# Kernel optimization log

Hardware: AMD Instinct MI355X
Metric: run time of the kernel (lower is better)

Reference implementation:

```python
import jax, jax.numpy as jnp
import numpy as np

N_NODES = 150000   # node_num
N_CENTROIDS = 256  # in_feats (must equal out_feats per source view())
EMBED = 256        # out_feats
EPS = 1e-7


def setup_inputs() -> dict:
    key = jax.random.key(0)
    k1, k2, k3 = jax.random.split(key, 3)
    x = jax.random.normal(k1, (N_NODES, EMBED), dtype=jnp.float32)
    # project node representations strictly inside the unit Poincare ball
    x = x / (1.0 + jnp.linalg.norm(x, axis=-1, keepdims=True)) * 0.9
    mask = (jax.random.uniform(k2, (N_NODES, 1)) < 0.9).astype(jnp.float32)
    # centroid_embedding init: uniform(-0.01, 0.01), already well inside the ball
    w = jax.random.uniform(k3, (N_CENTROIDS, EMBED), minval=-0.01, maxval=0.01,
                           dtype=jnp.float32)
    return {"node_repr": x, "mask": mask, "centroid_weight": w}


def _poincare_pairwise(x, c):
    # x: [N, D] inside unit ball, c: [C, D] inside unit ball -> [N, C]
    sx = jnp.sum(x * x, axis=-1)              # [N]
    sc = jnp.sum(c * c, axis=-1)              # [C]
    xc = x @ c.T                               # [N, C] (the only GEMM)
    sq = jnp.maximum(sx[:, None] + sc[None, :] - 2.0 * xc, 0.0)  # ||x-y||^2
    denom = jnp.maximum((1.0 - sx)[:, None] * (1.0 - sc)[None, :], 1e-12)
    arg = 1.0 + 2.0 * sq / denom
    return jnp.arccosh(jnp.maximum(arg, 1.0 + EPS))


def reference(node_repr, mask, centroid_weight):
    # node_repr: [N, D], mask: [N, 1], centroid_weight: [C, D]
    d = _poincare_pairwise(node_repr, centroid_weight)     # [N, C]
    node_centroid_dist = d[None, :, :] * mask              # [1, N, C] (mask broadcasts)
    graph_centroid_dist = jnp.sum(node_centroid_dist, axis=1) / jnp.sum(mask)  # [1, C]
    return graph_centroid_dist, node_centroid_dist
```

## Files before the change

kernel.cpp:

```cpp
#include <hip/hip_runtime.h>
#include <hip/hip_bf16.h>

#define N_NODES 150000
#define CDIM 256
#define DIM 256

typedef float f32x4 __attribute__((ext_vector_type(4)));
typedef short bf16x8 __attribute__((ext_vector_type(8)));
typedef unsigned short u16x4 __attribute__((ext_vector_type(4)));

#define WS_CB 0
#define WS_SC 131072
#define WS_GACC 132096
#define WS_MSUM 133120

__device__ __forceinline__ unsigned short f2bf(float f) {
  unsigned u = __float_as_uint(f);
  u += 0x7FFFu + ((u >> 16) & 1u);
  return (unsigned short)(u >> 16);
}

__global__ void cd_prep(const float* __restrict__ cw, const float* __restrict__ mask,
                        unsigned short* __restrict__ cb, float* __restrict__ sc,
                        float* __restrict__ msum) {
  int b = blockIdx.x;
  int t = threadIdx.x;
  int wave = t >> 6, lane = t & 63;
  __shared__ float red[4];
  if (b < CDIM) {
    float v = cw[b * DIM + t];
    cb[(size_t)(t >> 3) * (CDIM * 8) + b * 8 + (t & 7)] = f2bf(v);
    float ss = v * v;
    #pragma unroll
    for (int off = 32; off >= 1; off >>= 1) ss += __shfl_xor(ss, off);
    if (lane == 0) red[wave] = ss;
    __syncthreads();
    if (t == 0) sc[b] = red[0] + red[1] + red[2] + red[3];
  } else {
    int idx = (b - CDIM) * 256 + t;
    const int stride = 64 * 256;
    float s = 0.f;
    for (int i = idx; i < N_NODES; i += stride) s += mask[i];
    #pragma unroll
    for (int off = 32; off >= 1; off >>= 1) s += __shfl_xor(s, off);
    if (lane == 0) red[wave] = s;
    __syncthreads();
    if (t == 0) atomicAdd(msum, red[0] + red[1] + red[2] + red[3]);
  }
}

__global__ __launch_bounds__(256, 4)
void cd_main(const float* __restrict__ x, const float* __restrict__ mask,
             const unsigned short* __restrict__ cb, const float* __restrict__ sc,
             float* __restrict__ gacc, float* __restrict__ out1) {
  __shared__ unsigned short ab[32 * 64 * 8];
  __shared__ float sxl[64];

  const int t = threadIdx.x;
  const long m0 = (long)blockIdx.x * 64;

  {
    const int row = t >> 2;
    const int qq  = t & 3;
    const long grow = m0 + row;
    const bool ok = grow < N_NODES;
    const float* px = x + grow * DIM;
    float ss = 0.f;
    #pragma unroll
    for (int i = 0; i < 16; ++i) {
      const int col4 = qq * 4 + i * 16;
      f32x4 v;
      if (ok) v = *(const f32x4*)(px + col4);
      else    v = f32x4{0.f, 0.f, 0.f, 0.f};
      ss = fmaf(v.x, v.x, ss); ss = fmaf(v.y, v.y, ss);
      ss = fmaf(v.z, v.z, ss); ss = fmaf(v.w, v.w, ss);
      u16x4 b;
      b[0] = f2bf(v.x); b[1] = f2bf(v.y); b[2] = f2bf(v.z); b[3] = f2bf(v.w);
      *(u16x4*)(ab + ((size_t)(col4 >> 3) * 64 + row) * 8 + (col4 & 7)) = b;
    }
    ss += __shfl_xor(ss, 1);
    ss += __shfl_xor(ss, 2);
    if (qq == 0) sxl[row] = ss;
  }
  __syncthreads();

  const int lane = t & 63;
  const int w = t >> 6;
  const int q = lane >> 4;
  const int ln = lane & 15;
  const int c0 = w * 64;

  f32x4 acc[4][4] = {};
  #pragma unroll
  for (int kt = 0; kt < 8; ++kt) {
    bf16x8 bf[4];
    #pragma unroll
    for (int nt = 0; nt < 4; ++nt)
      bf[nt] = *(const bf16x8*)(cb + (size_t)(kt * 4 + q) * (CDIM * 8) + (c0 + nt * 16 + ln) * 8);
    #pragma unroll
    for (int mt = 0; mt < 4; ++mt) {
      bf16x8 af = *(const bf16x8*)(ab + ((size_t)(kt * 4 + q) * 64 + mt * 16 + ln) * 8);
      #pragma unroll
      for (int nt = 0; nt < 4; ++nt)
        acc[mt][nt] = __builtin_amdgcn_mfma_f32_16x16x32_bf16(af, bf[nt], acc[mt][nt], 0, 0, 0);
    }
  }

  float scv[4], rcv[4];
  #pragma unroll
  for (int nt = 0; nt < 4; ++nt) {
    scv[nt] = sc[c0 + nt * 16 + ln];
    rcv[nt] = 1.0f - scv[nt];
  }

  float pc[4] = {0.f, 0.f, 0.f, 0.f};
  #pragma unroll
  for (int mt = 0; mt < 4; ++mt) {
    float sxe[4], rxe[4], mke[4];
    long rows[4];
    #pragma unroll
    for (int i = 0; i < 4; ++i) {
      const int rloc = q * 4 + i;
      sxe[i] = sxl[mt * 16 + rloc];
      rows[i] = m0 + mt * 16 + rloc;
      mke[i] = (rows[i] < N_NODES) ? mask[rows[i]] : 0.f;
      rxe[i] = 1.0f - sxe[i];
    }
    #pragma unroll
    for (int nt = 0; nt < 4; ++nt) {
      const int col = c0 + nt * 16 + ln;
      #pragma unroll
      for (int i = 0; i < 4; ++i) {
        float xc = acc[mt][nt][i];
        float sq = fmaf(-2.0f, xc, sxe[i] + scv[nt]);
        sq = fmaxf(sq, 0.0f);
        float den = fmaxf(rxe[i] * rcv[nt], 1e-12f);
        float z = 1.0f + __fdividef(2.0f * sq, den);
        z = fmaxf(z, 1.0f + 1e-7f);
        float t2 = z + sqrtf(fmaf(z, z, -1.0f));
        float dd = __log2f(t2) * 0.6931471805599453f;
        float o = dd * mke[i];
        if (rows[i] < N_NODES) out1[rows[i] * CDIM + col] = o;
        pc[nt] += o;
      }
    }
  }

  #pragma unroll
  for (int nt = 0; nt < 4; ++nt) {
    float s = pc[nt];
    s += __shfl_xor(s, 16);
    s += __shfl_xor(s, 32);
    if (lane < 16) atomicAdd(gacc + c0 + nt * 16 + ln, s);
  }
}

__global__ void cd_final(const float* __restrict__ gacc, const float* __restrict__ msum,
                         float* __restrict__ out0) {
  int t = threadIdx.x;
  out0[t] = gacc[t] / msum[0];
}

extern "C" void kernel_launch(void* const* d_in, const int* in_sizes, int n_in,
                              void* d_out, int out_size, void* d_ws, size_t ws_size,
                              hipStream_t stream) {
  const float* x    = (const float*)d_in[0];
  const float* mask = (const float*)d_in[1];
  const float* cw   = (const float*)d_in[2];
  float* out = (float*)d_out;
  char* ws = (char*)d_ws;
  unsigned short* cb = (unsigned short*)(ws + WS_CB);
  float* sc   = (float*)(ws + WS_SC);
  float* gacc = (float*)(ws + WS_GACC);
  float* msum = (float*)(ws + WS_MSUM);

  hipMemsetAsync(ws + WS_GACC, 0, 256 * 4 + 4, stream);
  cd_prep<<<320, 256, 0, stream>>>(cw, mask, cb, sc, msum);
  const int nblocks = (N_NODES + 63) / 64;
  cd_main<<<nblocks, 256, 0, stream>>>(x, mask, cb, sc, gacc, out + 256);
  cd_final<<<1, 256, 0, stream>>>(gacc, msum, out);
}
```

Before: 327.9 us.

## Shrink row tile to 32, prefetch centroid fragments, precompute reciprocal denominators

```diff
diff --git a/kernel.cpp b/kernel.cpp
--- a/kernel.cpp
+++ b/kernel.cpp
@@ -4,6 +4,7 @@
 #define N_NODES 150000
 #define CDIM 256
 #define DIM 256
+#define BM 32
 
 typedef float f32x4 __attribute__((ext_vector_type(4)));
 typedef short bf16x8 __attribute__((ext_vector_type(8)));
@@ -11,8 +12,9 @@
 
 #define WS_CB 0
 #define WS_SC 131072
-#define WS_GACC 132096
-#define WS_MSUM 133120
+#define WS_RC2 132096
+#define WS_GACC 133120
+#define WS_MSUM 134144
 
 __device__ __forceinline__ unsigned short f2bf(float f) {
   unsigned u = __float_as_uint(f);
@@ -22,7 +24,7 @@
 
 __global__ void cd_prep(const float* __restrict__ cw, const float* __restrict__ mask,
                         unsigned short* __restrict__ cb, float* __restrict__ sc,
-                        float* __restrict__ msum) {
+                        float* __restrict__ rc2, float* __restrict__ msum) {
   int b = blockIdx.x;
   int t = threadIdx.x;
   int wave = t >> 6, lane = t & 63;
@@ -35,7 +37,11 @@
     for (int off = 32; off >= 1; off >>= 1) ss += __shfl_xor(ss, off);
     if (lane == 0) red[wave] = ss;
     __syncthreads();
-    if (t == 0) sc[b] = red[0] + red[1] + red[2] + red[3];
+    if (t == 0) {
+      float s = red[0] + red[1] + red[2] + red[3];
+      sc[b] = s;
+      rc2[b] = 2.0f / (1.0f - s);
+    }
   } else {
     int idx = (b - CDIM) * 256 + t;
     const int stride = 64 * 256;
@@ -52,35 +58,43 @@
 __global__ __launch_bounds__(256, 4)
 void cd_main(const float* __restrict__ x, const float* __restrict__ mask,
              const unsigned short* __restrict__ cb, const float* __restrict__ sc,
-             float* __restrict__ gacc, float* __restrict__ out1) {
-  __shared__ unsigned short ab[32 * 64 * 8];
-  __shared__ float sxl[64];
+             const float* __restrict__ rc2, float* __restrict__ gacc,
+             float* __restrict__ out1) {
+  __shared__ unsigned short ab[32 * BM * 8];
+  __shared__ float sxl[BM];
+  __shared__ float mskl[BM];
 
   const int t = threadIdx.x;
-  const long m0 = (long)blockIdx.x * 64;
+  const long m0 = (long)blockIdx.x * BM;
 
   {
-    const int row = t >> 2;
-    const int qq  = t & 3;
+    const int row = t >> 3;
+    const int sub = t & 7;
     const long grow = m0 + row;
     const bool ok = grow < N_NODES;
-    const float* px = x + grow * DIM;
+    const float* px = x + grow * DIM + sub * 4;
+    f32x4 v[8];
+    #pragma unroll
+    for (int i = 0; i < 8; ++i)
+      v[i] = ok ? *(const f32x4*)(px + i * 32) : f32x4{0.f, 0.f, 0.f, 0.f};
     float ss = 0.f;
     #pragma unroll
-    for (int i = 0; i < 16; ++i) {
-      const int col4 = qq * 4 + i * 16;
-      f32x4 v;
-      if (ok) v = *(const f32x4*)(px + col4);
-      else    v = f32x4{0.f, 0.f, 0.f, 0.f};
-      ss = fmaf(v.x, v.x, ss); ss = fmaf(v.y, v.y, ss);
-      ss = fmaf(v.z, v.z, ss); ss = fmaf(v.w, v.w, ss);
+    for (int i = 0; i < 8; ++i) {
+      ss = fmaf(v[i].x, v[i].x, ss); ss = fmaf(v[i].y, v[i].y, ss);
+      ss = fmaf(v[i].z, v[i].z, ss); ss = fmaf(v[i].w, v[i].w, ss);
       u16x4 b;
-      b[0] = f2bf(v.x); b[1] = f2bf(v.y); b[2] = f2bf(v.z); b[3] = f2bf(v.w);
-      *(u16x4*)(ab + ((size_t)(col4 >> 3) * 64 + row) * 8 + (col4 & 7)) = b;
+      b[0] = f2bf(v[i].x); b[1] = f2bf(v[i].y);
+      b[2] = f2bf(v[i].z); b[3] = f2bf(v[i].w);
+      const int kf = (sub >> 1) + i * 4;
+      *(u16x4*)(ab + ((size_t)kf * BM + row) * 8 + (sub & 1) * 4) = b;
     }
     ss += __shfl_xor(ss, 1);
     ss += __shfl_xor(ss, 2);
-    if (qq == 0) sxl[row] = ss;
+    ss += __shfl_xor(ss, 4);
+    if (sub == 0) {
+      sxl[row] = ss;
+      mskl[row] = ok ? mask[grow] : 0.f;
+    }
   }
   __syncthreads();
 
@@ -90,41 +104,52 @@
   const int ln = lane & 15;
   const int c0 = w * 64;
 
-  f32x4 acc[4][4] = {};
+  bf16x8 bfc[4], bfn[4];
+  #pragma unroll
+  for (int nt = 0; nt < 4; ++nt)
+    bfc[nt] = *(const bf16x8*)(cb + (size_t)q * (CDIM * 8) + (c0 + nt * 16 + ln) * 8);
+
+  f32x4 acc[2][4] = {};
   #pragma unroll
   for (int kt = 0; kt < 8; ++kt) {
-    bf16x8 bf[4];
-    #pragma unroll
-    for (int nt = 0; nt < 4; ++nt)
-      bf[nt] = *(const bf16x8*)(cb + (size_t)(kt * 4 + q) * (CDIM * 8) + (c0 + nt * 16 + ln) * 8);
-    #pragma unroll
-    for (int mt = 0; mt < 4; ++mt) {
-      bf16x8 af = *(const bf16x8*)(ab + ((size_t)(kt * 4 + q) * 64 + mt * 16 + ln) * 8);
+    if (kt < 7) {
       #pragma unroll
       for (int nt = 0; nt < 4; ++nt)
-        acc[mt][nt] = __builtin_amdgcn_mfma_f32_16x16x32_bf16(af, bf[nt], acc[mt][nt], 0, 0, 0);
-    }
-  }
-
-  float scv[4], rcv[4];
+        bfn[nt] = *(const bf16x8*)(cb + (size_t)((kt + 1) * 4 + q) * (CDIM * 8) + (c0 + nt * 16 + ln) * 8);
+    }
+    bf16x8 af0 = *(const bf16x8*)(ab + ((size_t)(kt * 4 + q) * BM + ln) * 8);
+    bf16x8 af1 = *(const bf16x8*)(ab + ((size_t)(kt * 4 + q) * BM + 16 + ln) * 8);
+    #pragma unroll
+    for (int nt = 0; nt < 4; ++nt)
+      acc[0][nt] = __builtin_amdgcn_mfma_f32_16x16x32_bf16(af0, bfc[nt], acc[0][nt], 0, 0, 0);
+    #pragma unroll
+    for (int nt = 0; nt < 4; ++nt)
+      acc[1][nt] = __builtin_amdgcn_mfma_f32_16x16x32_bf16(af1, bfc[nt], acc[1][nt], 0, 0, 0);
+    if (kt < 7) {
+      #pragma unroll
+      for (int nt = 0; nt < 4; ++nt) bfc[nt] = bfn[nt];
+    }
+  }
+
+  float scv[4], rc2v[4];
   #pragma unroll
   for (int nt = 0; nt < 4; ++nt) {
     scv[nt] = sc[c0 + nt * 16 + ln];
-    rcv[nt] = 1.0f - scv[nt];
+    rc2v[nt] = rc2[c0 + nt * 16 + ln];
   }
 
   float pc[4] = {0.f, 0.f, 0.f, 0.f};
   #pragma unroll
-  for (int mt = 0; mt < 4; ++mt) {
-    float sxe[4], rxe[4], mke[4];
+  for (int mt = 0; mt < 2; ++mt) {
+    float sxe[4], rxi[4], mke[4];
     long rows[4];
     #pragma unroll
     for (int i = 0; i < 4; ++i) {
-      const int rloc = q * 4 + i;
-      sxe[i] = sxl[mt * 16 + rloc];
-      rows[i] = m0 + mt * 16 + rloc;
-      mke[i] = (rows[i] < N_NODES) ? mask[rows[i]] : 0.f;
-      rxe[i] = 1.0f - sxe[i];
+      const int rloc = mt * 16 + q * 4 + i;
+      sxe[i] = sxl[rloc];
+      rows[i] = m0 + rloc;
+      mke[i] = mskl[rloc] * 0.6931471805599453f;
+      rxi[i] = __builtin_amdgcn_rcpf(1.0f - sxe[i]);
     }
     #pragma unroll
     for (int nt = 0; nt < 4; ++nt) {
@@ -132,14 +157,11 @@
       #pragma unroll
       for (int i = 0; i < 4; ++i) {
         float xc = acc[mt][nt][i];
-        float sq = fmaf(-2.0f, xc, sxe[i] + scv[nt]);
-        sq = fmaxf(sq, 0.0f);
-        float den = fmaxf(rxe[i] * rcv[nt], 1e-12f);
-        float z = 1.0f + __fdividef(2.0f * sq, den);
+        float sq = fmaxf(fmaf(-2.0f, xc, sxe[i] + scv[nt]), 0.0f);
+        float z = fmaf(sq * rxi[i], rc2v[nt], 1.0f);
         z = fmaxf(z, 1.0f + 1e-7f);
         float t2 = z + sqrtf(fmaf(z, z, -1.0f));
-        float dd = __log2f(t2) * 0.6931471805599453f;
-        float o = dd * mke[i];
+        float o = __log2f(t2) * mke[i];
         if (rows[i] < N_NODES) out1[rows[i] * CDIM + col] = o;
         pc[nt] += o;
       }
@@ -171,12 +193,13 @@
   char* ws = (char*)d_ws;
   unsigned short* cb = (unsigned short*)(ws + WS_CB);
   float* sc   = (float*)(ws + WS_SC);
+  float* rc2  = (float*)(ws + WS_RC2);
   float* gacc = (float*)(ws + WS_GACC);
   float* msum = (float*)(ws + WS_MSUM);
 
   hipMemsetAsync(ws + WS_GACC, 0, 256 * 4 + 4, stream);
-  cd_prep<<<320, 256, 0, stream>>>(cw, mask, cb, sc, msum);
-  const int nblocks = (N_NODES + 63) / 64;
-  cd_main<<<nblocks, 256, 0, stream>>>(x, mask, cb, sc, gacc, out + 256);
+  cd_prep<<<320, 256, 0, stream>>>(cw, mask, cb, sc, rc2, msum);
+  const int nblocks = (N_NODES + BM - 1) / BM;
+  cd_main<<<nblocks, 256, 0, stream>>>(x, mask, cb, sc, rc2, gacc, out + 256);
   cd_final<<<1, 256, 0, stream>>>(gacc, msum, out);
 }
```

New measurement: 340.3 us. 3.8% more time.
